# Kernel optimization log

Measured on AMD Instinct MI355X. Metric: run time of the kernel, lower is better.

## Reference

```python
import jax, jax.numpy as jnp
import numpy as np

B, S, E, H = 2, 2048, 1024, 16
D = E // H  # head_dim = 64


def setup_inputs() -> dict:
    key = jax.random.key(0)
    ks = jax.random.split(key, 8)
    lim = float(np.sqrt(6.0 / (E + E)))  # xavier_uniform
    inp = {
        "query": jax.random.normal(ks[0], (B, S, E), jnp.float32),
        "key": jax.random.normal(ks[1], (B, S, E), jnp.float32),
        "value": jax.random.normal(ks[2], (B, S, E), jnp.float32),
        "Wq": jax.random.uniform(ks[3], (E, E), jnp.float32, -lim, lim),
        "Wk": jax.random.uniform(ks[4], (E, E), jnp.float32, -lim, lim),
        "Wv": jax.random.uniform(ks[5], (E, E), jnp.float32, -lim, lim),
        "Wo": jax.random.uniform(ks[6], (E, E), jnp.float32, -lim, lim),
        "bq": jnp.zeros((E,), jnp.float32),
        "bk": jnp.zeros((E,), jnp.float32),
        "bv": jnp.zeros((E,), jnp.float32),
        "bo": jnp.zeros((E,), jnp.float32),
        # causal mask: True = masked (strictly upper triangular)
        "attn_mask": jnp.triu(jnp.ones((S, S), jnp.bool_), k=1),
    }
    return inp


def reference(query, key, value, Wq, Wk, Wv, Wo, bq, bk, bv, bo, attn_mask):
    # W stored as (in, out); torch Linear equivalent y = x @ W + b
    scaling = D ** (-0.5)
    q = (query @ Wq + bq) * scaling            # (B,S,E), first scaling (MHA.forward)
    k = key @ Wk + bk
    v = value @ Wv + bv
    # split heads -> (B, H, S, D)
    q = q.reshape(B, S, H, D).transpose(0, 2, 1, 3)
    k = k.reshape(B, S, H, D).transpose(0, 2, 1, 3)
    v = v.reshape(B, S, H, D).transpose(0, 2, 1, 3)
    # second scaling inside ScaledDotProductAttention (faithful double-scale)
    scores = jnp.einsum("bhqd,bhkd->bhqk", q, k) / jnp.sqrt(jnp.float32(D))
    scores = jnp.where(attn_mask[None, None, :, :], -jnp.inf, scores)
    attn = jax.nn.softmax(scores, axis=-1)     # dropout is identity in eval
    out = jnp.einsum("bhqk,bhkd->bhqd", attn, v)
    out = out.transpose(0, 2, 1, 3).reshape(B, S, E)
    return out @ Wo + bo
```

## Files before the change

### kernel.cpp

```cpp
#include <hip/hip_runtime.h>
#include <stdint.h>

#define B_ 2
#define S_ 2048
#define E_ 1024
#define H_ 16
#define D_ 64

typedef __attribute__((ext_vector_type(8))) short bf16x8;
typedef __attribute__((ext_vector_type(4))) float f32x4;
typedef __attribute__((ext_vector_type(4))) short s16x4_t;

__device__ __forceinline__ short bfbits(float x) {
    union { float f; uint32_t u; } v; v.f = x;
    uint32_t r = v.u + 0x7fffu + ((v.u >> 16) & 1u);
    return (short)(r >> 16);
}
__device__ __forceinline__ short bfbits_trunc(float x) {
    union { float f; uint32_t u; } v; v.f = x;
    return (short)(v.u >> 16);
}

__device__ __forceinline__ void async16(const short* g, short* l) {
    __builtin_amdgcn_global_load_lds((const __attribute__((address_space(1))) void*)g,
                                     (__attribute__((address_space(3))) void*)l,
                                     16, 0, 0);
}

__global__ __launch_bounds__(256) void cvt_inputs(const float* __restrict__ q,
                                                  const float* __restrict__ k,
                                                  const float* __restrict__ v,
                                                  short* __restrict__ dst) {
    const long long NV = 1048576;
    long long i = (long long)blockIdx.x * 256 + threadIdx.x;
    const float* src = (i < NV) ? q : (i < 2 * NV) ? k : v;
    long long j = (i >= 2 * NV) ? (i - 2 * NV) : (i >= NV) ? (i - NV) : i;
    float4 x = ((const float4*)src)[j];
    s16x4_t o;
    o[0] = bfbits(x.x); o[1] = bfbits(x.y); o[2] = bfbits(x.z); o[3] = bfbits(x.w);
    ((s16x4_t*)dst)[i] = o;
}

__global__ __launch_bounds__(256) void cvt_wT(const float* __restrict__ Wq,
                                              const float* __restrict__ Wk,
                                              const float* __restrict__ Wv,
                                              const float* __restrict__ Wo,
                                              short* __restrict__ dst) {
    __shared__ short t[64][72];
    int z = blockIdx.z;
    const float* W = (z == 0) ? Wq : (z == 1) ? Wk : (z == 2) ? Wv : Wo;
    short* o = dst + (size_t)z * 1048576;
    int n0 = blockIdx.x * 64, k0 = blockIdx.y * 64;
    int tid = threadIdx.x;
    int r = tid >> 4, c4 = tid & 15;
    for (int rep = 0; rep < 4; rep++) {
        int kk = rep * 16 + r;
        float4 x = *(const float4*)&W[(size_t)(k0 + kk) * 1024 + n0 + c4 * 4];
        t[c4 * 4 + 0][kk] = bfbits(x.x);
        t[c4 * 4 + 1][kk] = bfbits(x.y);
        t[c4 * 4 + 2][kk] = bfbits(x.z);
        t[c4 * 4 + 3][kk] = bfbits(x.w);
    }
    __syncthreads();
    int n = tid >> 3, c8 = tid & 7;
    for (int rep = 0; rep < 2; rep++) {
        int nn = rep * 32 + n;
        bf16x8 vv;
        for (int jj = 0; jj < 8; jj++) vv[jj] = t[nn][c8 * 8 + jj];
        *(bf16x8*)&o[(size_t)(n0 + nn) * 1024 + k0 + c8 * 8] = vv;
    }
}

__device__ __forceinline__ void gemm_core(const short* __restrict__ A,
                                          const short* __restrict__ Bt,
                                          const float* __restrict__ bias,
                                          short* __restrict__ outB,
                                          float* __restrict__ outF,
                                          int mode, float scale,
                                          int m0, int n0) {
    __shared__ short As[2][128 * 32];
    __shared__ short Bs[2][128 * 32];
    int tid = threadIdx.x, lane = tid & 63, w = tid >> 6;
    int col = lane & 15, quad = lane >> 4;
    int wm = (w >> 1) * 64, wn = (w & 1) * 64;
    f32x4 acc[4][4];
    for (int i = 0; i < 4; i++)
        for (int j = 0; j < 4; j++) acc[i][j] = (f32x4){0.f, 0.f, 0.f, 0.f};

    int r4 = lane >> 2;
    int skoff = ((lane & 3) ^ ((r4 >> 1) & 3)) * 8;
    const short* ga = A + (size_t)(m0 + r4) * 1024 + skoff;
    const short* gb = Bt + (size_t)(n0 + r4) * 1024 + skoff;

    int fro = (quad ^ ((col >> 1) & 3)) * 8;

    auto stage = [&](int t, int b) {
        int k0_ = t * 32;
        for (int c = 0; c < 2; ++c) {
            int rb = w * 32 + c * 16;
            async16(ga + (size_t)rb * 1024 + k0_, &As[b][rb * 32]);
            async16(gb + (size_t)rb * 1024 + k0_, &Bs[b][rb * 32]);
        }
    };

    stage(0, 0);
    __syncthreads();
    for (int t = 0; t < 32; ++t) {
        int cur = t & 1;
        if (t + 1 < 32) stage(t + 1, cur ^ 1);
        bf16x8 af[4], bfr[4];
        for (int i = 0; i < 4; i++)
            af[i] = *(const bf16x8*)&As[cur][(wm + i * 16 + col) * 32 + fro];
        for (int j = 0; j < 4; j++)
            bfr[j] = *(const bf16x8*)&Bs[cur][(wn + j * 16 + col) * 32 + fro];
        for (int i = 0; i < 4; i++)
            for (int j = 0; j < 4; j++)
                acc[i][j] = __builtin_amdgcn_mfma_f32_16x16x32_bf16(af[i], bfr[j], acc[i][j], 0, 0, 0);
        __syncthreads();
    }

    int mbase = m0 + wm + quad * 4;
    for (int i = 0; i < 4; i++) {
        int mb = mbase + i * 16;
        for (int j = 0; j < 4; j++) {
            int n = n0 + wn + j * 16 + col;
            float bv_ = bias[n];
            if (mode == 0) {
                for (int r = 0; r < 4; r++)
                    outB[(size_t)(mb + r) * 1024 + n] = bfbits((acc[i][j][r] + bv_) * scale);
            } else if (mode == 1) {
                int b_ = mb >> 11, s_ = mb & 2047;
                size_t base = (((size_t)(b_ * 16 + (n >> 6)) * 64) + (n & 63)) * 2048 + s_;
                s16x4_t pv;
                for (int r = 0; r < 4; r++) pv[r] = bfbits((acc[i][j][r] + bv_) * scale);
                *(s16x4_t*)&outB[base] = pv;
            } else {
                for (int r = 0; r < 4; r++)
                    outF[(size_t)(mb + r) * 1024 + n] = (acc[i][j][r] + bv_) * scale;
            }
        }
    }
}

#define QSCALE (0.015625f * 1.44269504088896340736f)
__global__ __launch_bounds__(256) void gemm_qkv(const short* __restrict__ Xb,
                                                const short* __restrict__ Wb,
                                                const float* __restrict__ bq,
                                                const float* __restrict__ bk,
                                                const float* __restrict__ bv,
                                                short* __restrict__ Qp) {
    int bid = blockIdx.x;
    int L = (bid & 7) * 96 + (bid >> 3);
    int z = L >> 8;
    int rem = L & 255;
    int m0 = (rem >> 3) * 128, n0 = (rem & 7) * 128;
    const short* A = Xb + (size_t)z * 4194304;
    const short* Bt = Wb + (size_t)z * 1048576;
    const float* bias = (z == 0) ? bq : (z == 1) ? bk : bv;
    short* outB = Qp + (size_t)z * 4194304;
    gemm_core(A, Bt, bias, outB, nullptr, (z == 2) ? 1 : 0, (z == 0) ? QSCALE : 1.0f,
              m0, n0);
}

__global__ __launch_bounds__(256) void gemm_o(const short* __restrict__ Ctx,
                                              const short* __restrict__ Wob,
                                              const float* __restrict__ bo,
                                              float* __restrict__ out) {
    int bid = blockIdx.x;
    int L = (bid & 7) * 32 + (bid >> 3);
    int m0 = (L >> 3) * 128, n0 = (L & 7) * 128;
    gemm_core(Ctx, Wob, bo, nullptr, out, 2, 1.0f, m0, n0);
}

__device__ __forceinline__ void stage_kv(const short* __restrict__ Kp,
                                         const short* __restrict__ VpT,
                                         short* Kbuf, short* Vbuf,
                                         int b, int bh, int h, int kv0,
                                         int lane, int w) {
    int r8 = lane >> 3;
    int sk = ((lane & 7) ^ r8) * 8;
    for (int c = 0; c < 2; c++) {
        int rb = (c * 4 + w) * 8;
        async16(Kp + (size_t)(b * 2048 + kv0 + rb + r8) * 1024 + h * 64 + sk,
                &Kbuf[rb * 64]);
        async16(VpT + (size_t)(bh * 64 + rb + r8) * 2048 + kv0 + sk,
                &Vbuf[rb * 64]);
    }
}

__global__ __launch_bounds__(256) void attn_kernel(const short* __restrict__ Qp,
                                                   const short* __restrict__ Kp,
                                                   const short* __restrict__ VpT,
                                                   short* __restrict__ Ctx) {
    __shared__ short Kt[2][64 * 64];
    __shared__ short Vt[2][64 * 64];
    __shared__ short Pl[4][16 * 72];
    int tid = threadIdx.x, lane = tid & 63, w = tid >> 6;
    int col = lane & 15, quad = lane >> 4;
    int c7 = col & 7;
    int bid = blockIdx.x;
    int L = (bid & 7) * 64 + (bid >> 3);
    int qx = L & 15, bh = L >> 4;
    int b = bh >> 4, h = bh & 15;

    bf16x8 ones;
    for (int j = 0; j < 8; j++) ones[j] = (short)0x3F80;

    for (int half = 0; half < 2; half++) {
        int qt = half ? (31 - qx) : qx;
        int qrow = qt * 64 + w * 16;

        bf16x8 aq0, aq1;
        {
            const short* qa = Qp + ((size_t)(b * 2048 + qrow + col)) * 1024 + h * 64;
            aq0 = *(const bf16x8*)(qa + quad * 8);
            aq1 = *(const bf16x8*)(qa + 32 + quad * 8);
        }
        f32x4 o[4];
        for (int dj = 0; dj < 4; dj++) o[dj] = (f32x4){0.f, 0.f, 0.f, 0.f};
        f32x4 psv = (f32x4){0.f, 0.f, 0.f, 0.f};

        int n = qt + 1;
        if (half) __syncthreads();
        stage_kv(Kp, VpT, Kt[0], Vt[0], b, bh, h, 0, lane, w);

        for (int t = 0; t < n; t++) {
            __syncthreads();
            if (t + 1 < n)
                stage_kv(Kp, VpT, Kt[(t + 1) & 1], Vt[(t + 1) & 1], b, bh, h,
                         (t + 1) * 64, lane, w);
            const short* Kb = Kt[t & 1];
            const short* Vb = Vt[t & 1];

            f32x4 sf[4];
            for (int i = 0; i < 4; i++) sf[i] = (f32x4){0.f, 0.f, 0.f, 0.f};
            __builtin_amdgcn_s_setprio(1);
            for (int ks = 0; ks < 2; ks++) {
                bf16x8 bq_ = ks ? aq1 : aq0;
                int sl = ((ks * 4 + quad) ^ c7) * 8;
                for (int i = 0; i < 4; i++) {
                    bf16x8 ak_ = *(const bf16x8*)&Kb[(i * 16 + col) * 64 + sl];
                    sf[i] = __builtin_amdgcn_mfma_f32_16x16x32_bf16(ak_, bq_, sf[i], 0, 0, 0);
                }
            }
            __builtin_amdgcn_s_setprio(0);
            if (t == n - 1) {
                int qg = qrow + col;
                for (int i = 0; i < 4; i++) {
                    int kvg = t * 64 + i * 16 + quad * 4;
                    for (int r = 0; r < 4; r++)
                        if (kvg + r > qg) sf[i][r] = -3.0e38f;
                }
            }
            for (int i = 0; i < 4; i++) {
                s16x4_t pw;
                for (int r = 0; r < 4; r++)
                    pw[r] = bfbits_trunc(exp2f(sf[i][r]));
                *(s16x4_t*)&Pl[w][col * 72 + i * 16 + quad * 4] = pw;
            }
            __builtin_amdgcn_s_setprio(1);
            for (int ks = 0; ks < 2; ks++) {
                bf16x8 ap = *(const bf16x8*)&Pl[w][col * 72 + ks * 32 + quad * 8];
                int sl = ((ks * 4 + quad) ^ c7) * 8;
                psv = __builtin_amdgcn_mfma_f32_16x16x32_bf16(ap, ones, psv, 0, 0, 0);
                for (int dj = 0; dj < 4; dj++) {
                    bf16x8 bv_ = *(const bf16x8*)&Vb[(dj * 16 + col) * 64 + sl];
                    o[dj] = __builtin_amdgcn_mfma_f32_16x16x32_bf16(ap, bv_, o[dj], 0, 0, 0);
                }
            }
            __builtin_amdgcn_s_setprio(0);
        }
        float inv[4];
        for (int r = 0; r < 4; r++) inv[r] = 1.0f / psv[r];
        for (int r = 0; r < 4; r++) {
            for (int dj = 0; dj < 4; dj++) {
                float val = o[dj][r] * inv[r];
                Ctx[((size_t)(b * 2048 + qrow + quad * 4 + r)) * 1024 + h * 64 + dj * 16 + col] = bfbits(val);
            }
        }
    }
}

extern "C" void kernel_launch(void* const* d_in, const int* in_sizes, int n_in,
                              void* d_out, int out_size, void* d_ws, size_t ws_size,
                              hipStream_t stream) {
    const float* q  = (const float*)d_in[0];
    const float* k  = (const float*)d_in[1];
    const float* v  = (const float*)d_in[2];
    const float* Wq = (const float*)d_in[3];
    const float* Wk = (const float*)d_in[4];
    const float* Wv = (const float*)d_in[5];
    const float* Wo = (const float*)d_in[6];
    const float* bq = (const float*)d_in[7];
    const float* bk = (const float*)d_in[8];
    const float* bv = (const float*)d_in[9];
    const float* bo = (const float*)d_in[10];

    short* wsb = (short*)d_ws;
    short* Wb  = wsb;
    short* Xb  = Wb + 4 * 1048576;
    short* Qp  = Xb + 3 * 4194304;
    short* Kp  = Qp + 4194304;
    short* VpT = Kp + 4194304;
    short* Ctx = VpT + 4194304;

    cvt_inputs<<<12288, 256, 0, stream>>>(q, k, v, Xb);
    cvt_wT<<<dim3(16, 16, 4), 256, 0, stream>>>(Wq, Wk, Wv, Wo, Wb);
    gemm_qkv<<<768, 256, 0, stream>>>(Xb, Wb, bq, bk, bv, Qp);
    attn_kernel<<<512, 256, 0, stream>>>(Qp, Kp, VpT, Ctx);
    gemm_o<<<256, 256, 0, stream>>>(Ctx, Wb + 3 * 1048576, bo, (float*)d_out);
}
```

Measured before the change: 239.6 us.

## Merge conversion kernels and give each attention block one query tile, longest first

Merges the input and weight conversion kernels into a single launch to save one kernel launch. The attention kernel previously paired a short and a long causal query tile per block (512 blocks). It now launches 1024 blocks, one tile each, ordered so the longest tiles are dispatched first. This relies on the hardware scheduler for load balance instead of static pairing, and Q tiles and K/V staging are now set up per block.

```diff
diff --git a/kernel.cpp b/kernel.cpp
--- a/kernel.cpp
+++ b/kernel.cpp
@@ -27,30 +27,34 @@
                                      16, 0, 0);
 }
 
-__global__ __launch_bounds__(256) void cvt_inputs(const float* __restrict__ q,
-                                                  const float* __restrict__ k,
-                                                  const float* __restrict__ v,
-                                                  short* __restrict__ dst) {
-    const long long NV = 1048576;
-    long long i = (long long)blockIdx.x * 256 + threadIdx.x;
-    const float* src = (i < NV) ? q : (i < 2 * NV) ? k : v;
-    long long j = (i >= 2 * NV) ? (i - 2 * NV) : (i >= NV) ? (i - NV) : i;
-    float4 x = ((const float4*)src)[j];
-    s16x4_t o;
-    o[0] = bfbits(x.x); o[1] = bfbits(x.y); o[2] = bfbits(x.z); o[3] = bfbits(x.w);
-    ((s16x4_t*)dst)[i] = o;
-}
-
-__global__ __launch_bounds__(256) void cvt_wT(const float* __restrict__ Wq,
-                                              const float* __restrict__ Wk,
-                                              const float* __restrict__ Wv,
-                                              const float* __restrict__ Wo,
-                                              short* __restrict__ dst) {
+__global__ __launch_bounds__(256) void cvt_all(const float* __restrict__ q,
+                                               const float* __restrict__ k,
+                                               const float* __restrict__ v,
+                                               const float* __restrict__ Wq,
+                                               const float* __restrict__ Wk,
+                                               const float* __restrict__ Wv,
+                                               const float* __restrict__ Wo,
+                                               short* __restrict__ dstX,
+                                               short* __restrict__ dstW) {
     __shared__ short t[64][72];
-    int z = blockIdx.z;
+    int bid = blockIdx.x;
+    if (bid < 12288) {
+        const long long NV = 1048576;
+        long long i = (long long)bid * 256 + threadIdx.x;
+        const float* src = (i < NV) ? q : (i < 2 * NV) ? k : v;
+        long long j = (i >= 2 * NV) ? (i - 2 * NV) : (i >= NV) ? (i - NV) : i;
+        float4 x = ((const float4*)src)[j];
+        s16x4_t o;
+        o[0] = bfbits(x.x); o[1] = bfbits(x.y); o[2] = bfbits(x.z); o[3] = bfbits(x.w);
+        ((s16x4_t*)dstX)[i] = o;
+        return;
+    }
+    int wbid = bid - 12288;
+    int z = wbid >> 8;
     const float* W = (z == 0) ? Wq : (z == 1) ? Wk : (z == 2) ? Wv : Wo;
-    short* o = dst + (size_t)z * 1048576;
-    int n0 = blockIdx.x * 64, k0 = blockIdx.y * 64;
+    short* o = dstW + (size_t)z * 1048576;
+    int rem = wbid & 255;
+    int n0 = (rem & 15) * 64, k0 = (rem >> 4) * 64;
     int tid = threadIdx.x;
     int r = tid >> 4, c4 = tid & 15;
     for (int rep = 0; rep < 4; rep++) {
@@ -199,84 +203,80 @@
     int col = lane & 15, quad = lane >> 4;
     int c7 = col & 7;
     int bid = blockIdx.x;
-    int L = (bid & 7) * 64 + (bid >> 3);
-    int qx = L & 15, bh = L >> 4;
+    int L = (bid & 7) * 128 + (bid >> 3);
+    int bh = L >> 5;
+    int qt = 31 - (L & 31);
     int b = bh >> 4, h = bh & 15;
+    int qrow = qt * 64 + w * 16;
 
     bf16x8 ones;
     for (int j = 0; j < 8; j++) ones[j] = (short)0x3F80;
 
-    for (int half = 0; half < 2; half++) {
-        int qt = half ? (31 - qx) : qx;
-        int qrow = qt * 64 + w * 16;
-
-        bf16x8 aq0, aq1;
-        {
-            const short* qa = Qp + ((size_t)(b * 2048 + qrow + col)) * 1024 + h * 64;
-            aq0 = *(const bf16x8*)(qa + quad * 8);
-            aq1 = *(const bf16x8*)(qa + 32 + quad * 8);
-        }
-        f32x4 o[4];
-        for (int dj = 0; dj < 4; dj++) o[dj] = (f32x4){0.f, 0.f, 0.f, 0.f};
-        f32x4 psv = (f32x4){0.f, 0.f, 0.f, 0.f};
-
-        int n = qt + 1;
-        if (half) __syncthreads();
-        stage_kv(Kp, VpT, Kt[0], Vt[0], b, bh, h, 0, lane, w);
-
-        for (int t = 0; t < n; t++) {
-            __syncthreads();
-            if (t + 1 < n)
-                stage_kv(Kp, VpT, Kt[(t + 1) & 1], Vt[(t + 1) & 1], b, bh, h,
-                         (t + 1) * 64, lane, w);
-            const short* Kb = Kt[t & 1];
-            const short* Vb = Vt[t & 1];
-
-            f32x4 sf[4];
-            for (int i = 0; i < 4; i++) sf[i] = (f32x4){0.f, 0.f, 0.f, 0.f};
-            __builtin_amdgcn_s_setprio(1);
-            for (int ks = 0; ks < 2; ks++) {
-                bf16x8 bq_ = ks ? aq1 : aq0;
-                int sl = ((ks * 4 + quad) ^ c7) * 8;
-                for (int i = 0; i < 4; i++) {
-                    bf16x8 ak_ = *(const bf16x8*)&Kb[(i * 16 + col) * 64 + sl];
-                    sf[i] = __builtin_amdgcn_mfma_f32_16x16x32_bf16(ak_, bq_, sf[i], 0, 0, 0);
-                }
+    bf16x8 aq0, aq1;
+    {
+        const short* qa = Qp + ((size_t)(b * 2048 + qrow + col)) * 1024 + h * 64;
+        aq0 = *(const bf16x8*)(qa + quad * 8);
+        aq1 = *(const bf16x8*)(qa + 32 + quad * 8);
+    }
+    f32x4 o[4];
+    for (int dj = 0; dj < 4; dj++) o[dj] = (f32x4){0.f, 0.f, 0.f, 0.f};
+    f32x4 psv = (f32x4){0.f, 0.f, 0.f, 0.f};
+
+    int n = qt + 1;
+    stage_kv(Kp, VpT, Kt[0], Vt[0], b, bh, h, 0, lane, w);
+
+    for (int t = 0; t < n; t++) {
+        __syncthreads();
+        if (t + 1 < n)
+            stage_kv(Kp, VpT, Kt[(t + 1) & 1], Vt[(t + 1) & 1], b, bh, h,
+                     (t + 1) * 64, lane, w);
+        const short* Kb = Kt[t & 1];
+        const short* Vb = Vt[t & 1];
+
+        f32x4 sf[4];
+        for (int i = 0; i < 4; i++) sf[i] = (f32x4){0.f, 0.f, 0.f, 0.f};
+        __builtin_amdgcn_s_setprio(1);
+        for (int ks = 0; ks < 2; ks++) {
+            bf16x8 bq_ = ks ? aq1 : aq0;
+            int sl = ((ks * 4 + quad) ^ c7) * 8;
+            for (int i = 0; i < 4; i++) {
+                bf16x8 ak_ = *(const bf16x8*)&Kb[(i * 16 + col) * 64 + sl];
+                sf[i] = __builtin_amdgcn_mfma_f32_16x16x32_bf16(ak_, bq_, sf[i], 0, 0, 0);
             }
-            __builtin_amdgcn_s_setprio(0);
-            if (t == n - 1) {
-                int qg = qrow + col;
-                for (int i = 0; i < 4; i++) {
-                    int kvg = t * 64 + i * 16 + quad * 4;
-                    for (int r = 0; r < 4; r++)
-                        if (kvg + r > qg) sf[i][r] = -3.0e38f;
-                }
+        }
+        __builtin_amdgcn_s_setprio(0);
+        if (t == n - 1) {
+            int qg = qrow + col;
+            for (int i = 0; i < 4; i++) {
+                int kvg = t * 64 + i * 16 + quad * 4;
+                for (int r = 0; r < 4; r++)
+                    if (kvg + r > qg) sf[i][r] = -3.0e38f;
             }
-            for (int i = 0; i < 4; i++) {
-                s16x4_t pw;
-                for (int r = 0; r < 4; r++)
-                    pw[r] = bfbits_trunc(exp2f(sf[i][r]));
-                *(s16x4_t*)&Pl[w][col * 72 + i * 16 + quad * 4] = pw;
+        }
+        for (int i = 0; i < 4; i++) {
+            s16x4_t pw;
+            for (int r = 0; r < 4; r++)
+                pw[r] = bfbits_trunc(exp2f(sf[i][r]));
+            *(s16x4_t*)&Pl[w][col * 72 + i * 16 + quad * 4] = pw;
+        }
+        __builtin_amdgcn_s_setprio(1);
+        for (int ks = 0; ks < 2; ks++) {
+            bf16x8 ap = *(const bf16x8*)&Pl[w][col * 72 + ks * 32 + quad * 8];
+            int sl = ((ks * 4 + quad) ^ c7) * 8;
+            psv = __builtin_amdgcn_mfma_f32_16x16x32_bf16(ap, ones, psv, 0, 0, 0);
+            for (int dj = 0; dj < 4; dj++) {
+                bf16x8 bv_ = *(const bf16x8*)&Vb[(dj * 16 + col) * 64 + sl];
+                o[dj] = __builtin_amdgcn_mfma_f32_16x16x32_bf16(ap, bv_, o[dj], 0, 0, 0);
             }
-            __builtin_amdgcn_s_setprio(1);
-            for (int ks = 0; ks < 2; ks++) {
-                bf16x8 ap = *(const bf16x8*)&Pl[w][col * 72 + ks * 32 + quad * 8];
-                int sl = ((ks * 4 + quad) ^ c7) * 8;
-                psv = __builtin_amdgcn_mfma_f32_16x16x32_bf16(ap, ones, psv, 0, 0, 0);
-                for (int dj = 0; dj < 4; dj++) {
-                    bf16x8 bv_ = *(const bf16x8*)&Vb[(dj * 16 + col) * 64 + sl];
-                    o[dj] = __builtin_amdgcn_mfma_f32_16x16x32_bf16(ap, bv_, o[dj], 0, 0, 0);
-                }
-            }
-            __builtin_amdgcn_s_setprio(0);
-        }
-        float inv[4];
-        for (int r = 0; r < 4; r++) inv[r] = 1.0f / psv[r];
-        for (int r = 0; r < 4; r++) {
-            for (int dj = 0; dj < 4; dj++) {
-                float val = o[dj][r] * inv[r];
-                Ctx[((size_t)(b * 2048 + qrow + quad * 4 + r)) * 1024 + h * 64 + dj * 16 + col] = bfbits(val);
-            }
+        }
+        __builtin_amdgcn_s_setprio(0);
+    }
+    float inv[4];
+    for (int r = 0; r < 4; r++) inv[r] = 1.0f / psv[r];
+    for (int r = 0; r < 4; r++) {
+        for (int dj = 0; dj < 4; dj++) {
+            float val = o[dj][r] * inv[r];
+            Ctx[((size_t)(b * 2048 + qrow + quad * 4 + r)) * 1024 + h * 64 + dj * 16 + col] = bfbits(val);
         }
     }
 }
@@ -304,9 +304,8 @@
     short* VpT = Kp + 4194304;
     short* Ctx = VpT + 4194304;
 
-    cvt_inputs<<<12288, 256, 0, stream>>>(q, k, v, Xb);
-    cvt_wT<<<dim3(16, 16, 4), 256, 0, stream>>>(Wq, Wk, Wv, Wo, Wb);
+    cvt_all<<<13312, 256, 0, stream>>>(q, k, v, Wq, Wk, Wv, Wo, Xb, Wb);
     gemm_qkv<<<768, 256, 0, stream>>>(Xb, Wb, bq, bk, bv, Qp);
-    attn_kernel<<<512, 256, 0, stream>>>(Qp, Kp, VpT, Ctx);
+    attn_kernel<<<1024, 256, 0, stream>>>(Qp, Kp, VpT, Ctx);
     gemm_o<<<256, 256, 0, stream>>>(Ctx, Wb + 3 * 1048576, bo, (float*)d_out);
 }
```

Result: slower. 245.3 us (+2.4%).
